# Performance work log

Measured on AMD Instinct MI355X. Metric: run time of the kernel, lower is better.

## Reference

```python
import jax, jax.numpy as jnp
import numpy as np

L, N, DIN, DOUT = 24, 8192, 256, 128  # levels, nodes/level, dim_in(=2*dim_out), dim_out


def setup_inputs() -> dict:
    key = jax.random.key(0)
    ks = jax.random.split(key, 6)
    s = 1.0 / np.sqrt(DIN)
    tensor = jax.random.normal(ks[0], (L, N, DIN), jnp.float32)
    # child indices into previous level's nodes; -1 == missing child -> learned init state
    indices = jax.random.randint(ks[1], (L, N, 2), -1, N).astype(jnp.int32)
    W_w = jax.random.uniform(ks[2], (4 * DOUT, DIN), jnp.float32, -s, s)
    W_b = jax.random.uniform(ks[3], (4 * DOUT,), jnp.float32, -s, s)
    U_f1 = jax.random.uniform(ks[4], (DOUT, 2 * DOUT), jnp.float32, -s, s)
    U_f2 = jax.random.uniform(jax.random.fold_in(ks[4], 1), (DOUT, 2 * DOUT), jnp.float32, -s, s)
    U_iuo = jax.random.uniform(ks[5], (3 * DOUT, 2 * DOUT), jnp.float32, -s, s)
    h_init = jnp.zeros((1, DOUT), jnp.float32)
    c_init = jnp.zeros((1, DOUT), jnp.float32)
    return dict(tensor=tensor, indices=indices, h_init=h_init, c_init=c_init,
                W_w=W_w, W_b=W_b, U_f1=U_f1, U_f2=U_f2, U_iuo=U_iuo)


def reference(tensor, indices, h_init, c_init, W_w, W_b, U_f1, U_f2, U_iuo):
    D = DOUT

    def step(carry, inp):
        h_prev, c_prev = carry                      # [N, D] each (previous level)
        x, idx = inp                                # x:[N,DIN], idx:[N,2]
        h_ext = jnp.concatenate([h_init, h_prev], axis=0)  # row 0 = init (index -1)
        c_ext = jnp.concatenate([c_init, c_prev], axis=0)
        rows = idx + 1                              # -1 -> 0 (init state)
        h = h_ext[rows]                             # [N, 2, D] gathered child hiddens
        c = c_ext[rows]                             # [N, 2, D]
        W_x = x @ W_w.T + W_b                       # [N, 4D]
        f_x, i_x, u_x, o_x = jnp.split(W_x, 4, axis=1)
        hc = h.reshape(h.shape[0], 2 * D)           # [N, 2D]
        f1 = jax.nn.sigmoid(f_x + hc @ U_f1.T)
        f2 = jax.nn.sigmoid(f_x + hc @ U_f2.T)
        iuo = hc @ U_iuo.T                          # [N, 3D]
        i = jax.nn.sigmoid(iuo[:, :D] + i_x)
        u = jnp.tanh(iuo[:, D:2 * D] + u_x)
        o = jax.nn.sigmoid(iuo[:, 2 * D:] + o_x)
        new_c = i * u + f1 * c[:, 0] + f2 * c[:, 1]
        new_h = o * jnp.tanh(new_c)
        return (new_h, new_c), (new_h, new_c)

    n = tensor.shape[1]
    h0 = jnp.broadcast_to(h_init, (n, D))
    c0 = jnp.broadcast_to(c_init, (n, D))
    _, (res_h, res_c) = jax.lax.scan(step, (h0, c0), (tensor, indices))
    return res_h, res_c                              # each [L, N, D]
```

## Files before the change

kernel.cpp:

```cpp
#include <hip/hip_runtime.h>
#include <stdint.h>

#define LVL 24
#define NN  8192
#define DIN 256
#define DD  128
#define BM  16

typedef __attribute__((ext_vector_type(8))) short bf16x8;
typedef __attribute__((ext_vector_type(4))) float f32x4;

__device__ __forceinline__ float b2f(unsigned short u) {
    union { unsigned int i; float f; } v; v.i = ((unsigned int)u) << 16; return v.f;
}
__device__ __forceinline__ unsigned short f2b(float f) {
    union { float f; unsigned int i; } v; v.f = f;
    unsigned int x = v.i;
    return (unsigned short)((x + 0x7fffu + ((x >> 16) & 1u)) >> 16);
}
__device__ __forceinline__ float sig_(float x) { return 1.0f / (1.0f + __expf(-x)); }

__device__ __forceinline__ float ldf(const void* p, size_t i, int isf) {
    return isf ? ((const float*)p)[i] : b2f(((const unsigned short*)p)[i]);
}

__global__ void detect_kernel(const unsigned short* __restrict__ t, int* __restrict__ flag) {
    __shared__ int cnt;
    if (threadIdx.x == 0) cnt = 0;
    __syncthreads();
    int bad = 0;
    #pragma unroll
    for (int r = 0; r < 4; ++r) {
        unsigned short u = t[(threadIdx.x * 4 + r) * 2];
        int e = (u >> 7) & 255;
        bad += (e >= 136 || (e >= 1 && e <= 90)) ? 1 : 0;
    }
    atomicAdd(&cnt, bad);
    __syncthreads();
    if (threadIdx.x == 0) *flag = (cnt > 16) ? 1 : 0;
}

__global__ __launch_bounds__(256)
void convert_kernel(const void* Ww, const void* Wb, const void* Uf1, const void* Uf2,
                    const void* Uiuo, const void* hini, const void* cini,
                    unsigned short* __restrict__ wpack, float* __restrict__ bias,
                    unsigned short* __restrict__ hinit_b, float* __restrict__ cinit_f,
                    const int* __restrict__ flag) {
    const int isf = *flag;
    const int bid = blockIdx.x;
    const int t = threadIdx.x;
    if (bid < 1152) {
        const int row = bid, col = t;
        float v;
        if (row < 512)       v = ldf(Ww,   (size_t)row * DIN + col, isf);
        else if (row < 640)  v = ldf(Uf1,  (size_t)(row - 512) * DIN + col, isf);
        else if (row < 768)  v = ldf(Uf2,  (size_t)(row - 640) * DIN + col, isf);
        else                 v = ldf(Uiuo, (size_t)(row - 768) * DIN + col, isf);
        const int g  = row >> 7;
        const int wr = row & 127;
        const int dt = wr >> 4;
        const int mm = wr & 15;
        const int kk = col >> 5;
        const int q  = (col >> 3) & 3;
        const int j  = col & 7;
        const size_t pos = (size_t)((g * 8 + dt) * 8 + kk) * 512 + (q * 16 + mm) * 8 + j;
        wpack[pos] = f2b(v);
    } else if (bid == 1152) {
        bias[t] = ldf(Wb, t, isf);
    } else if (bid == 1153) {
        bias[256 + t] = ldf(Wb, 256 + t, isf);
    } else {
        if (t < 128) hinit_b[t] = f2b(ldf(hini, t, isf));
        else if (t < 256) cinit_f[t - 128] = ldf(cini, t - 128, isf);
    }
}

__global__ __launch_bounds__(512, 4)
void level_kernel(const void* __restrict__ xbase, int level,
                  const int* __restrict__ idx,
                  const unsigned short* __restrict__ hprev,
                  const float* __restrict__ cprev,
                  unsigned short* __restrict__ hnew,
                  float* __restrict__ outh,
                  float* __restrict__ outc,
                  const unsigned short* __restrict__ wpack,
                  const float* __restrict__ bias,
                  const unsigned short* __restrict__ hinit_b,
                  const float* __restrict__ cinit_f,
                  const int* __restrict__ flag,
                  int first) {
    __shared__ unsigned short xs[4096];
    __shared__ unsigned short hs[4096];
    __shared__ float cs[32 * 132];

    const int tid = threadIdx.x;
    const int isf = *flag;
    const int bm  = blockIdx.x;

    {
        const int u = tid >> 4;
        const int r = tid & 15;
        const int kk = u >> 2, q = u & 3;
        const size_t re = (size_t)level * NN * DIN + (size_t)(bm * BM + r) * DIN + u * 8;
        union { unsigned short us[8]; uint4 v; } t;
        if (isf) {
            const float4* xr = (const float4*)((const float*)xbase + re);
            float4 v0 = xr[0], v1 = xr[1];
            t.us[0] = f2b(v0.x); t.us[1] = f2b(v0.y); t.us[2] = f2b(v0.z); t.us[3] = f2b(v0.w);
            t.us[4] = f2b(v1.x); t.us[5] = f2b(v1.y); t.us[6] = f2b(v1.z); t.us[7] = f2b(v1.w);
        } else {
            t.v = *(const uint4*)((const unsigned short*)xbase + re);
        }
        *(uint4*)&xs[kk * 512 + q * 128 + r * 8] = t.v;
    }

    {
        const int r    = tid & 15;
        const int s    = (tid >> 4) & 1;
        const int part = tid >> 5;
        const int ai = idx[(bm * BM + r) * 2 + s];
        const int use_init = (first || ai < 0);

        const unsigned short* hsrc = use_init ? (hinit_b + part * 8)
                                              : (hprev + (size_t)ai * DD + part * 8);
        uint4 hv = *(const uint4*)hsrc;
        const int col = s * 128 + part * 8;
        const int kk = col >> 5, q = (col >> 3) & 3;
        *(uint4*)&hs[kk * 512 + q * 128 + r * 8] = hv;

        const float* csrc = use_init ? (cinit_f + part * 8)
                                     : (cprev + (size_t)ai * DD + part * 8);
        float4 c0 = ((const float4*)csrc)[0];
        float4 c1 = ((const float4*)csrc)[1];
        float* cdst = &cs[(s * 16 + r) * 132 + part * 8];
        ((float4*)cdst)[0] = c0;
        ((float4*)cdst)[1] = c1;
    }
    __syncthreads();

    const int lane = tid & 63;
    const int dt   = tid >> 6;
    const int m    = lane & 15;
    const int q    = lane >> 4;
    const int d    = dt * 16 + m;

    const unsigned short* wb = wpack + (size_t)dt * 4096 + (size_t)lane * 8;

    f32x4 acc[9];
    #pragma unroll
    for (int g = 0; g < 9; ++g) acc[g] = (f32x4)0.0f;

    #pragma unroll
    for (int kk = 0; kk < 8; ++kk) {
        const int xo = kk * 512 + q * 128 + m * 8;
        bf16x8 a = *(const bf16x8*)&xs[xo];
        bf16x8 h = *(const bf16x8*)&hs[xo];
        #pragma unroll
        for (int g = 0; g < 4; ++g) {
            bf16x8 b = *(const bf16x8*)(wb + (size_t)g * 32768 + kk * 512);
            acc[g] = __builtin_amdgcn_mfma_f32_16x16x32_bf16(a, b, acc[g], 0, 0, 0);
        }
        #pragma unroll
        for (int g = 4; g < 9; ++g) {
            bf16x8 b = *(const bf16x8*)(wb + (size_t)g * 32768 + kk * 512);
            acc[g] = __builtin_amdgcn_mfma_f32_16x16x32_bf16(h, b, acc[g], 0, 0, 0);
        }
    }

    const float bfv = bias[d], biv = bias[128 + d], buv = bias[256 + d], bov = bias[384 + d];
    #pragma unroll
    for (int j = 0; j < 4; ++j) {
        const int rr = q * 4 + j;
        const int nd = bm * BM + rr;
        const float ca = cs[rr * 132 + d];
        const float cb = cs[(16 + rr) * 132 + d];
        const float fx = acc[0][j] + bfv;
        const float ix = acc[1][j] + biv;
        const float ux = acc[2][j] + buv;
        const float ox = acc[3][j] + bov;
        const float f1 = sig_(fx + acc[4][j]);
        const float f2 = sig_(fx + acc[5][j]);
        const float ig = sig_(ix + acc[6][j]);
        const float ug = tanhf(ux + acc[7][j]);
        const float og = sig_(ox + acc[8][j]);
        const float nc = ig * ug + f1 * ca + f2 * cb;
        const float nh = og * tanhf(nc);
        const size_t o = (size_t)nd * DD + d;
        hnew[o] = f2b(nh);
        outh[o] = nh;
        outc[o] = nc;
    }
}

extern "C" void kernel_launch(void* const* d_in, const int* in_sizes, int n_in,
                              void* d_out, int out_size, void* d_ws, size_t ws_size,
                              hipStream_t stream) {
    const void* tensor  = d_in[0];
    const int*  indices = (const int*)d_in[1];
    const void* h_init  = d_in[2];
    const void* c_init  = d_in[3];
    const void* Ww      = d_in[4];
    const void* Wb      = d_in[5];
    const void* Uf1     = d_in[6];
    const void* Uf2     = d_in[7];
    const void* Uiuo    = d_in[8];
    float* out = (float*)d_out;

    char* wsb = (char*)d_ws;
    int* flag                = (int*)wsb;
    unsigned short* wpack    = (unsigned short*)(wsb + 256);
    float* bias              = (float*)(wsb + 590336);
    unsigned short* hinit_b  = (unsigned short*)(wsb + 592640);
    float* cinit_f           = (float*)(wsb + 593152);
    unsigned short* hb0      = (unsigned short*)(wsb + (1u << 20));
    unsigned short* hb1      = (unsigned short*)(wsb + (1u << 20) + 2097152);

    detect_kernel<<<1, 64, 0, stream>>>((const unsigned short*)tensor, flag);
    convert_kernel<<<1155, 256, 0, stream>>>(Ww, Wb, Uf1, Uf2, Uiuo, h_init, c_init,
                                             wpack, bias, hinit_b, cinit_f, flag);

    unsigned short* hp = hb0;
    unsigned short* hn = hb1;
    for (int l = 0; l < LVL; ++l) {
        const float* cprev = (l == 0) ? (const float*)out
                                      : (const float*)(out + (size_t)(LVL + l - 1) * NN * DD);
        level_kernel<<<NN / BM, 512, 0, stream>>>(
            tensor, l,
            indices + (size_t)l * NN * 2,
            hp, cprev, hn,
            out + (size_t)l * NN * DD,
            out + (size_t)(LVL + l) * NN * DD,
            wpack, bias, hinit_b, cinit_f, flag, (l == 0) ? 1 : 0);
        unsigned short* th = hp; hp = hn; hn = th;
    }
}
```

Baseline: 769.9 us.

## Retile level kernel to 32-row blocks split over two output-column halves

Each block now covers 32 nodes and half of the output columns, using 256 threads (4 waves), with a 2D grid. Each wave issues two MFMAs per weight fragment, so every B-operand load is reused across two 16-row tiles, halving weight traffic per node. The price is that x and h tiles are loaded by both column-half blocks, LDS use roughly doubles, and the accumulator register count doubles, which may lower occupancy.

```diff
diff --git a/kernel.cpp b/kernel.cpp
--- a/kernel.cpp
+++ b/kernel.cpp
@@ -5,7 +5,7 @@
 #define NN  8192
 #define DIN 256
 #define DD  128
-#define BM  16
+#define BM  32
 
 typedef __attribute__((ext_vector_type(8))) short bf16x8;
 typedef __attribute__((ext_vector_type(4))) float f32x4;
@@ -75,7 +75,7 @@
     }
 }
 
-__global__ __launch_bounds__(512, 4)
+__global__ __launch_bounds__(256, 3)
 void level_kernel(const void* __restrict__ xbase, int level,
                   const int* __restrict__ idx,
                   const unsigned short* __restrict__ hprev,
@@ -89,106 +89,124 @@
                   const float* __restrict__ cinit_f,
                   const int* __restrict__ flag,
                   int first) {
-    __shared__ unsigned short xs[4096];
-    __shared__ unsigned short hs[4096];
-    __shared__ float cs[32 * 132];
+    __shared__ unsigned short xs[8192];
+    __shared__ unsigned short hs[8192];
+    __shared__ float cs[64 * 68];
 
     const int tid = threadIdx.x;
     const int isf = *flag;
     const int bm  = blockIdx.x;
+    const int yh  = blockIdx.y;
 
     {
-        const int u = tid >> 4;
-        const int r = tid & 15;
-        const int kk = u >> 2, q = u & 3;
-        const size_t re = (size_t)level * NN * DIN + (size_t)(bm * BM + r) * DIN + u * 8;
-        union { unsigned short us[8]; uint4 v; } t;
-        if (isf) {
-            const float4* xr = (const float4*)((const float*)xbase + re);
-            float4 v0 = xr[0], v1 = xr[1];
-            t.us[0] = f2b(v0.x); t.us[1] = f2b(v0.y); t.us[2] = f2b(v0.z); t.us[3] = f2b(v0.w);
-            t.us[4] = f2b(v1.x); t.us[5] = f2b(v1.y); t.us[6] = f2b(v1.z); t.us[7] = f2b(v1.w);
-        } else {
-            t.v = *(const uint4*)((const unsigned short*)xbase + re);
-        }
-        *(uint4*)&xs[kk * 512 + q * 128 + r * 8] = t.v;
+        const int u0 = tid >> 4;
+        const int r0 = tid & 15;
+        #pragma unroll
+        for (int du = 0; du < 2; ++du) {
+            const int u = u0 + du * 16;
+            const int kk = u >> 2, q = u & 3;
+            #pragma unroll
+            for (int dr = 0; dr < 2; ++dr) {
+                const int r = r0 + dr * 16;
+                const size_t re = (size_t)level * NN * DIN + (size_t)(bm * BM + r) * DIN + u * 8;
+                union { unsigned short us[8]; uint4 v; } t;
+                if (isf) {
+                    const float4* xr = (const float4*)((const float*)xbase + re);
+                    float4 v0 = xr[0], v1 = xr[1];
+                    t.us[0] = f2b(v0.x); t.us[1] = f2b(v0.y); t.us[2] = f2b(v0.z); t.us[3] = f2b(v0.w);
+                    t.us[4] = f2b(v1.x); t.us[5] = f2b(v1.y); t.us[6] = f2b(v1.z); t.us[7] = f2b(v1.w);
+                } else {
+                    t.v = *(const uint4*)((const unsigned short*)xbase + re);
+                }
+                *(uint4*)&xs[kk * 1024 + q * 256 + r * 8] = t.v;
+            }
+        }
     }
 
     {
-        const int r    = tid & 15;
-        const int s    = (tid >> 4) & 1;
-        const int part = tid >> 5;
+        const int r  = tid & 31;
+        const int sp = tid >> 5;
+        const int s    = sp >> 2;
+        const int part = sp & 3;
         const int ai = idx[(bm * BM + r) * 2 + s];
         const int use_init = (first || ai < 0);
 
-        const unsigned short* hsrc = use_init ? (hinit_b + part * 8)
-                                              : (hprev + (size_t)ai * DD + part * 8);
-        uint4 hv = *(const uint4*)hsrc;
-        const int col = s * 128 + part * 8;
-        const int kk = col >> 5, q = (col >> 3) & 3;
-        *(uint4*)&hs[kk * 512 + q * 128 + r * 8] = hv;
-
-        const float* csrc = use_init ? (cinit_f + part * 8)
-                                     : (cprev + (size_t)ai * DD + part * 8);
-        float4 c0 = ((const float4*)csrc)[0];
-        float4 c1 = ((const float4*)csrc)[1];
-        float* cdst = &cs[(s * 16 + r) * 132 + part * 8];
-        ((float4*)cdst)[0] = c0;
-        ((float4*)cdst)[1] = c1;
+        const unsigned short* hsrc = use_init ? (hinit_b + part * 32)
+                                              : (hprev + (size_t)ai * DD + part * 32);
+        const int kk = s * 4 + part;
+        #pragma unroll
+        for (int q = 0; q < 4; ++q)
+            *(uint4*)&hs[kk * 1024 + q * 256 + r * 8] = ((const uint4*)hsrc)[q];
+
+        const float* csrc = use_init ? (cinit_f + yh * 64 + part * 16)
+                                     : (cprev + (size_t)ai * DD + yh * 64 + part * 16);
+        float* cdst = &cs[(s * 32 + r) * 68 + part * 16];
+        #pragma unroll
+        for (int q = 0; q < 4; ++q)
+            ((float4*)cdst)[q] = ((const float4*)csrc)[q];
     }
     __syncthreads();
 
     const int lane = tid & 63;
-    const int dt   = tid >> 6;
+    const int wave = tid >> 6;
     const int m    = lane & 15;
     const int q    = lane >> 4;
-    const int d    = dt * 16 + m;
+    const int dt   = yh * 4 + wave;
+    const int d    = yh * 64 + wave * 16 + m;
 
     const unsigned short* wb = wpack + (size_t)dt * 4096 + (size_t)lane * 8;
 
-    f32x4 acc[9];
-    #pragma unroll
-    for (int g = 0; g < 9; ++g) acc[g] = (f32x4)0.0f;
+    f32x4 acc[9][2];
+    #pragma unroll
+    for (int g = 0; g < 9; ++g) { acc[g][0] = (f32x4)0.0f; acc[g][1] = (f32x4)0.0f; }
 
     #pragma unroll
     for (int kk = 0; kk < 8; ++kk) {
-        const int xo = kk * 512 + q * 128 + m * 8;
-        bf16x8 a = *(const bf16x8*)&xs[xo];
-        bf16x8 h = *(const bf16x8*)&hs[xo];
+        const int xo = kk * 1024 + q * 256 + m * 8;
+        bf16x8 a0 = *(const bf16x8*)&xs[xo];
+        bf16x8 a1 = *(const bf16x8*)&xs[xo + 128];
+        bf16x8 h0 = *(const bf16x8*)&hs[xo];
+        bf16x8 h1 = *(const bf16x8*)&hs[xo + 128];
         #pragma unroll
         for (int g = 0; g < 4; ++g) {
             bf16x8 b = *(const bf16x8*)(wb + (size_t)g * 32768 + kk * 512);
-            acc[g] = __builtin_amdgcn_mfma_f32_16x16x32_bf16(a, b, acc[g], 0, 0, 0);
+            acc[g][0] = __builtin_amdgcn_mfma_f32_16x16x32_bf16(a0, b, acc[g][0], 0, 0, 0);
+            acc[g][1] = __builtin_amdgcn_mfma_f32_16x16x32_bf16(a1, b, acc[g][1], 0, 0, 0);
         }
         #pragma unroll
         for (int g = 4; g < 9; ++g) {
             bf16x8 b = *(const bf16x8*)(wb + (size_t)g * 32768 + kk * 512);
-            acc[g] = __builtin_amdgcn_mfma_f32_16x16x32_bf16(h, b, acc[g], 0, 0, 0);
+            acc[g][0] = __builtin_amdgcn_mfma_f32_16x16x32_bf16(h0, b, acc[g][0], 0, 0, 0);
+            acc[g][1] = __builtin_amdgcn_mfma_f32_16x16x32_bf16(h1, b, acc[g][1], 0, 0, 0);
         }
     }
 
     const float bfv = bias[d], biv = bias[128 + d], buv = bias[256 + d], bov = bias[384 + d];
-    #pragma unroll
-    for (int j = 0; j < 4; ++j) {
-        const int rr = q * 4 + j;
-        const int nd = bm * BM + rr;
-        const float ca = cs[rr * 132 + d];
-        const float cb = cs[(16 + rr) * 132 + d];
-        const float fx = acc[0][j] + bfv;
-        const float ix = acc[1][j] + biv;
-        const float ux = acc[2][j] + buv;
-        const float ox = acc[3][j] + bov;
-        const float f1 = sig_(fx + acc[4][j]);
-        const float f2 = sig_(fx + acc[5][j]);
-        const float ig = sig_(ix + acc[6][j]);
-        const float ug = tanhf(ux + acc[7][j]);
-        const float og = sig_(ox + acc[8][j]);
-        const float nc = ig * ug + f1 * ca + f2 * cb;
-        const float nh = og * tanhf(nc);
-        const size_t o = (size_t)nd * DD + d;
-        hnew[o] = f2b(nh);
-        outh[o] = nh;
-        outc[o] = nc;
+    const int dloc = wave * 16 + m;
+    #pragma unroll
+    for (int mt = 0; mt < 2; ++mt) {
+        #pragma unroll
+        for (int j = 0; j < 4; ++j) {
+            const int rr = mt * 16 + q * 4 + j;
+            const int nd = bm * BM + rr;
+            const float ca = cs[rr * 68 + dloc];
+            const float cb = cs[(32 + rr) * 68 + dloc];
+            const float fx = acc[0][mt][j] + bfv;
+            const float ix = acc[1][mt][j] + biv;
+            const float ux = acc[2][mt][j] + buv;
+            const float ox = acc[3][mt][j] + bov;
+            const float f1 = sig_(fx + acc[4][mt][j]);
+            const float f2 = sig_(fx + acc[5][mt][j]);
+            const float ig = sig_(ix + acc[6][mt][j]);
+            const float ug = tanhf(ux + acc[7][mt][j]);
+            const float og = sig_(ox + acc[8][mt][j]);
+            const float nc = ig * ug + f1 * ca + f2 * cb;
+            const float nh = og * tanhf(nc);
+            const size_t o = (size_t)nd * DD + d;
+            hnew[o] = f2b(nh);
+            outh[o] = nh;
+            outc[o] = nc;
+        }
     }
 }
 
@@ -224,7 +242,7 @@
     for (int l = 0; l < LVL; ++l) {
         const float* cprev = (l == 0) ? (const float*)out
                                       : (const float*)(out + (size_t)(LVL + l - 1) * NN * DD);
-        level_kernel<<<NN / BM, 512, 0, stream>>>(
+        level_kernel<<<dim3(NN / BM, 2), 256, 0, stream>>>(
             tensor, l,
             indices + (size_t)l * NN * 2,
             hp, cprev, hn,
```

New measurement: 747.9 us. 2.9% less time.
